# Kernel tuning notes

Hardware: AMD Instinct MI355X
Metric: run time of the kernel (lower is better)

## Reference

```python
import jax, jax.numpy as jnp
import numpy as np

B, N, D, D_OUT = 4, 512, 48, 48

def setup_inputs() -> dict:
    key = jax.random.key(0)
    ks = jax.random.split(key, 7)
    s1 = 1.0 / np.sqrt(2 * D)
    s2 = 1.0 / np.sqrt(2 * D)
    s3 = 1.0 / np.sqrt(D)
    return {
        "x": jax.random.normal(ks[0], (B, N, D), dtype=jnp.float32),
        "W1": jax.random.uniform(ks[1], (2 * D, 2 * D), jnp.float32, -s1, s1),
        "b1": jax.random.uniform(ks[2], (2 * D,), jnp.float32, -s1, s1),
        "W2": jax.random.uniform(ks[3], (2 * D, D), jnp.float32, -s2, s2),
        "b2": jax.random.uniform(ks[4], (D,), jnp.float32, -s2, s2),
        "W3": jax.random.uniform(ks[5], (D, D_OUT), jnp.float32, -s3, s3),
        "b3": jax.random.uniform(ks[6], (D_OUT,), jnp.float32, -s3, s3),
    }

def reference(x, W1, b1, W2, b2, W3, b3):
    # x: [B, N, D]
    Bn, Nn, Dn = x.shape
    xi = jnp.broadcast_to(x[:, :, None, :], (Bn, Nn, Nn, Dn))  # row i
    xj = jnp.broadcast_to(x[:, None, :, :], (Bn, Nn, Nn, Dn))  # col j
    pair = jnp.concatenate([xi, xj], axis=-1)  # [B,N,N,2D]
    h = jax.nn.gelu(pair @ W1 + b1, approximate=False)
    h = jax.nn.gelu(h @ W2 + b2, approximate=False)
    pair_out = h @ W3 + b3  # [B,N,N,d_out]
    mask = jnp.triu(jnp.ones((Nn, Nn), dtype=bool), 1)  # j > i masked
    pair_out = jnp.where(mask[None, :, :, None], 0.0, pair_out)
    w = jnp.linalg.norm(pair_out, axis=-1)  # [B,N,N]
    w = jnp.where(mask[None, :, :], -1e9, w)
    w = jax.nn.softmax(w, axis=-1)
    return jnp.einsum('bnj,bnjd->bnd', w, pair_out)
```

## Files before the change

### kernel.cpp

```cpp
#include <hip/hip_runtime.h>
#include <hip/hip_bf16.h>


constexpr int BATCH = 4;
constexpr int SEQ   = 512;
constexpr int DIM   = 48;
constexpr int DIM2  = 96;
constexpr int CH    = 64;

constexpr int AW  = 104;
constexpr int HW  = 72;

typedef short short8v __attribute__((ext_vector_type(8)));
typedef float float4v __attribute__((ext_vector_type(4)));
typedef unsigned int uint2v __attribute__((ext_vector_type(2)));

#define MFMA16(a, b, c) __builtin_amdgcn_mfma_f32_16x16x32_bf16(a, b, c, 0, 0, 0)

__device__ __forceinline__ float gelu_tanh(float x) {
    float u = x * x;
    float q = fmaf(0.10294537f, u, 2.3022077f);
    float e = __builtin_amdgcn_exp2f(x * q);
    float r = __builtin_amdgcn_rcpf(e + 1.0f);
    return fmaf(-x, r, x);
}
__device__ __forceinline__ short f2bf1(float v) {
    return (short)((__float_as_uint(v) + 0x8000u) >> 16);
}
__device__ __forceinline__ unsigned pack_bf16x2(float a, float b) {
    unsigned ua = __float_as_uint(a) + 0x8000u;
    unsigned ub = __float_as_uint(b) + 0x8000u;
    return __builtin_amdgcn_perm(ub, ua, 0x07060302u);
}
constexpr float LOG2E = 1.4426950408889634f;

__global__ __launch_bounds__(192) void uv_kernel(
    const float* __restrict__ x, const float* __restrict__ W1,
    const float* __restrict__ b1, float* __restrict__ U, float* __restrict__ V)
{
    __shared__ float sxT[DIM * 4];
    const int t = threadIdx.x;
    const int row0 = blockIdx.x * 4;
    if (t < DIM * 4) {
        int r = t / DIM, m = t - r * DIM;
        sxT[m * 4 + r] = x[(row0 + r) * DIM + m];
    }
    __syncthreads();
    const bool isU = (t < DIM2);
    const int  k   = isU ? t : (t - DIM2);
    const float* Wcol = W1 + (isU ? 0 : DIM * DIM2) + k;
    float binit = isU ? b1[k] : 0.0f;
    float a0 = binit, a1 = binit, a2 = binit, a3 = binit;
    #pragma unroll 8
    for (int m = 0; m < DIM; ++m) {
        float wv = Wcol[m * DIM2];
        const float4 xa = *(const float4*)&sxT[m * 4];
        a0 = fmaf(wv, xa.x, a0); a1 = fmaf(wv, xa.y, a1);
        a2 = fmaf(wv, xa.z, a2); a3 = fmaf(wv, xa.w, a3);
    }
    float* dst = isU ? U : V;
    dst[(row0 + 0) * DIM2 + k] = a0; dst[(row0 + 1) * DIM2 + k] = a1;
    dst[(row0 + 2) * DIM2 + k] = a2; dst[(row0 + 3) * DIM2 + k] = a3;
}

__global__ __launch_bounds__(256, 4) void pair_kernel(
    const float* __restrict__ U, const float* __restrict__ V,
    const float* __restrict__ W2, const float* __restrict__ b2,
    const float* __restrict__ W3, const float* __restrict__ b3,
    float* __restrict__ out)
{
    __shared__ __align__(16) char smem[23168];
    short* sA   = (short*)smem;
    short* sH   = (short*)(smem + 13312);
    float* sUi  = (float*)(smem + 22528);
    float* sNrm = (float*)(smem + 22912);

    const int t   = threadIdx.x;
    const int bid = blockIdx.x;
    const int b   = bid & (BATCH - 1);
    const int i   = (SEQ - 1) - (bid >> 2);
    const int rowbase = b * SEQ + i;

    const int lane = t & 63;
    const int w    = t >> 6;
    const int col  = lane & 15;
    const int quad = lane >> 4;
    const int qo   = quad * 8;
    const int m4   = w * 16 + col;
    const int rbase = w * 16 + quad * 4;

    for (int idx = t; idx < DIM2 * DIM; idx += 256) {
        int k = idx / DIM, n = idx - k * DIM;
        sA[n * AW + k] = f2bf1(W2[idx]);
    }
    for (int idx = t; idx < DIM * DIM; idx += 256) {
        int k = idx / DIM, n = idx - k * DIM;
        sH[n * HW + k] = f2bf1(W3[idx]);
    }
    for (int idx = t; idx < CH * 16; idx += 256)
        sH[(idx >> 4) * HW + 48 + (idx & 15)] = 0;
    if (t < DIM2) sUi[t] = U[rowbase * DIM2 + t];
    __syncthreads();

    const short* w2b = sA + col * AW + qo;
    const short8v w200 = *(const short8v*)(w2b + 0);
    const short8v w201 = *(const short8v*)(w2b + 32);
    const short8v w202 = *(const short8v*)(w2b + 64);
    const short8v w210 = *(const short8v*)(w2b + 16*AW + 0);
    const short8v w211 = *(const short8v*)(w2b + 16*AW + 32);
    const short8v w212 = *(const short8v*)(w2b + 16*AW + 64);
    const short8v w220 = *(const short8v*)(w2b + 32*AW + 0);
    const short8v w221 = *(const short8v*)(w2b + 32*AW + 32);
    const short8v w222 = *(const short8v*)(w2b + 32*AW + 64);
    const short* w3b = sH + col * HW + qo;
    const short8v w300 = *(const short8v*)(w3b + 0);
    const short8v w301 = *(const short8v*)(w3b + 32);
    const short8v w310 = *(const short8v*)(w3b + 16*HW + 0);
    const short8v w311 = *(const short8v*)(w3b + 16*HW + 32);
    const short8v w320 = *(const short8v*)(w3b + 32*HW + 0);
    const short8v w321 = *(const short8v*)(w3b + 32*HW + 32);
    const float bb20 = b2[col], bb21 = b2[16 + col], bb22 = b2[32 + col];
    const float bb30 = b3[col], bb31 = b3[16 + col], bb32 = b3[32 + col];
    __syncthreads();

    const int pr = t >> 2;
    const int pq = t & 3;

    float acc0 = 0.f, acc1 = 0.f, acc2 = 0.f;
    float m_run = -1e30f, l_run = 0.0f;

    for (int j0 = 0; j0 <= i; j0 += CH) {
        const int JJ = min(CH, i + 1 - j0);

        {
            const float* Vb = V + (b * SEQ + j0 + pr) * DIM2 + pq * 4;
            #pragma unroll
            for (int kk = 0; kk < 6; ++kk) {
                const float4 vv = *(const float4*)(Vb + 16 * kk);
                const float4 uu = *(const float4*)&sUi[(pq + 4 * kk) * 4];
                float g0 = gelu_tanh(uu.x + vv.x);
                float g1 = gelu_tanh(uu.y + vv.y);
                float g2 = gelu_tanh(uu.z + vv.z);
                float g3 = gelu_tanh(uu.w + vv.w);
                uint2v o;
                o.x = pack_bf16x2(g0, g1);
                o.y = pack_bf16x2(g2, g3);
                *(uint2v*)&sA[pr * AW + (pq + 4 * kk) * 4] = o;
            }
        }
        __syncthreads();

        {
            const short* arow = &sA[m4 * AW + qo];
            short8v a0 = *(const short8v*)(arow + 0);
            short8v a1 = *(const short8v*)(arow + 32);
            short8v a2 = *(const short8v*)(arow + 64);
            float4v c0 = {0.f,0.f,0.f,0.f}, c1 = c0, c2 = c0;
            c0 = MFMA16(a0, w200, c0); c0 = MFMA16(a1, w201, c0); c0 = MFMA16(a2, w202, c0);
            c1 = MFMA16(a0, w210, c1); c1 = MFMA16(a1, w211, c1); c1 = MFMA16(a2, w212, c1);
            c2 = MFMA16(a0, w220, c2); c2 = MFMA16(a1, w221, c2); c2 = MFMA16(a2, w222, c2);
            #pragma unroll
            for (int r = 0; r < 4; ++r) {
                sH[(rbase + r) * HW +  0 + col] = f2bf1(gelu_tanh(c0[r] + bb20));
                sH[(rbase + r) * HW + 16 + col] = f2bf1(gelu_tanh(c1[r] + bb21));
                sH[(rbase + r) * HW + 32 + col] = f2bf1(gelu_tanh(c2[r] + bb22));
            }
        }
        __syncthreads();

        float4v p0, p1, p2;
        {
            const short* hrw = &sH[m4 * HW + qo];
            short8v a0 = *(const short8v*)(hrw + 0);
            short8v a1 = *(const short8v*)(hrw + 32);
            float4v c0 = {0.f,0.f,0.f,0.f}, c1 = c0, c2 = c0;
            c0 = MFMA16(a0, w300, c0); c0 = MFMA16(a1, w301, c0);
            c1 = MFMA16(a0, w310, c1); c1 = MFMA16(a1, w311, c1);
            c2 = MFMA16(a0, w320, c2); c2 = MFMA16(a1, w321, c2);
            #pragma unroll
            for (int r = 0; r < 4; ++r) {
                p0[r] = c0[r] + bb30; p1[r] = c1[r] + bb31; p2[r] = c2[r] + bb32;
                float ss = p0[r]*p0[r] + p1[r]*p1[r] + p2[r]*p2[r];
                ss += __shfl_xor(ss, 1);
                ss += __shfl_xor(ss, 2);
                ss += __shfl_xor(ss, 4);
                ss += __shfl_xor(ss, 8);
                if (col == 0) sNrm[rbase + r] = sqrtf(ss);
            }
        }
        __syncthreads();

        {
            float nr = (lane < JJ) ? sNrm[lane] : -1e30f;
            float mx = nr;
            mx = fmaxf(mx, __shfl_xor(mx, 1));  mx = fmaxf(mx, __shfl_xor(mx, 2));
            mx = fmaxf(mx, __shfl_xor(mx, 4));  mx = fmaxf(mx, __shfl_xor(mx, 8));
            mx = fmaxf(mx, __shfl_xor(mx, 16)); mx = fmaxf(mx, __shfl_xor(mx, 32));
            float newm = fmaxf(m_run, mx);
            float e = (lane < JJ) ? __builtin_amdgcn_exp2f((nr - newm) * LOG2E) : 0.0f;
            float s = e;
            s += __shfl_xor(s, 1);  s += __shfl_xor(s, 2);
            s += __shfl_xor(s, 4);  s += __shfl_xor(s, 8);
            s += __shfl_xor(s, 16); s += __shfl_xor(s, 32);
            float sc = __builtin_amdgcn_exp2f((m_run - newm) * LOG2E);
            l_run = fmaf(l_run, sc, s);
            m_run = newm;
            acc0 *= sc; acc1 *= sc; acc2 *= sc;
            #pragma unroll
            for (int r = 0; r < 4; ++r) {
                float er = __shfl(e, rbase + r);
                acc0 = fmaf(er, p0[r], acc0);
                acc1 = fmaf(er, p1[r], acc1);
                acc2 = fmaf(er, p2[r], acc2);
            }
        }
    }

    acc0 += __shfl_xor(acc0, 16); acc0 += __shfl_xor(acc0, 32);
    acc1 += __shfl_xor(acc1, 16); acc1 += __shfl_xor(acc1, 32);
    acc2 += __shfl_xor(acc2, 16); acc2 += __shfl_xor(acc2, 32);
    float* sRed = (float*)sA;
    __syncthreads();
    if (lane < 16) {
        sRed[w * DIM + lane]      = acc0;
        sRed[w * DIM + 16 + lane] = acc1;
        sRed[w * DIM + 32 + lane] = acc2;
    }
    __syncthreads();
    if (t < DIM) {
        float o = (sRed[t] + sRed[DIM + t] + sRed[2*DIM + t] + sRed[3*DIM + t]) / l_run;
        out[rowbase * DIM + t] = o;
    }
}

extern "C" void kernel_launch(void* const* d_in, const int* in_sizes, int n_in,
                              void* d_out, int out_size, void* d_ws, size_t ws_size,
                              hipStream_t stream) {
    const float* x  = (const float*)d_in[0];
    const float* W1 = (const float*)d_in[1];
    const float* b1 = (const float*)d_in[2];
    const float* W2 = (const float*)d_in[3];
    const float* b2 = (const float*)d_in[4];
    const float* W3 = (const float*)d_in[5];
    const float* b3 = (const float*)d_in[6];
    float* out = (float*)d_out;

    float* U = (float*)d_ws;
    float* V = U + BATCH * SEQ * DIM2;

    uv_kernel<<<BATCH * SEQ / 4, 192, 0, stream>>>(x, W1, b1, U, V);
    pair_kernel<<<BATCH * SEQ, 256, 0, stream>>>(U, V, W2, b2, W3, b3, out);
}
```

Baseline: 114.9 us.

## Use per-wave online softmax, skip inactive waves, keep W2 in LDS

```diff
diff --git a/kernel.cpp b/kernel.cpp
--- a/kernel.cpp
+++ b/kernel.cpp
@@ -14,6 +14,7 @@
 typedef short short8v __attribute__((ext_vector_type(8)));
 typedef float float4v __attribute__((ext_vector_type(4)));
 typedef unsigned int uint2v __attribute__((ext_vector_type(2)));
+typedef unsigned int uint4v __attribute__((ext_vector_type(4)));
 
 #define MFMA16(a, b, c) __builtin_amdgcn_mfma_f32_16x16x32_bf16(a, b, c, 0, 0, 0)
 
@@ -63,17 +64,16 @@
     dst[(row0 + 2) * DIM2 + k] = a2; dst[(row0 + 3) * DIM2 + k] = a3;
 }
 
-__global__ __launch_bounds__(256, 4) void pair_kernel(
+__global__ __launch_bounds__(256, 5) void pair_kernel(
     const float* __restrict__ U, const float* __restrict__ V,
     const float* __restrict__ W2, const float* __restrict__ b2,
     const float* __restrict__ W3, const float* __restrict__ b3,
     float* __restrict__ out)
 {
-    __shared__ __align__(16) char smem[23168];
+    __shared__ __align__(16) char smem[32512];
     short* sA   = (short*)smem;
-    short* sH   = (short*)(smem + 13312);
-    float* sUi  = (float*)(smem + 22528);
-    float* sNrm = (float*)(smem + 22912);
+    short* sW2T = (short*)(smem + 13312);
+    short* sH   = (short*)(smem + 23296);
 
     const int t   = threadIdx.x;
     const int bid = blockIdx.x;
@@ -91,7 +91,7 @@
 
     for (int idx = t; idx < DIM2 * DIM; idx += 256) {
         int k = idx / DIM, n = idx - k * DIM;
-        sA[n * AW + k] = f2bf1(W2[idx]);
+        sW2T[n * AW + k] = f2bf1(W2[idx]);
     }
     for (int idx = t; idx < DIM * DIM; idx += 256) {
         int k = idx / DIM, n = idx - k * DIM;
@@ -99,19 +99,18 @@
     }
     for (int idx = t; idx < CH * 16; idx += 256)
         sH[(idx >> 4) * HW + 48 + (idx & 15)] = 0;
-    if (t < DIM2) sUi[t] = U[rowbase * DIM2 + t];
-    __syncthreads();
-
-    const short* w2b = sA + col * AW + qo;
-    const short8v w200 = *(const short8v*)(w2b + 0);
-    const short8v w201 = *(const short8v*)(w2b + 32);
-    const short8v w202 = *(const short8v*)(w2b + 64);
-    const short8v w210 = *(const short8v*)(w2b + 16*AW + 0);
-    const short8v w211 = *(const short8v*)(w2b + 16*AW + 32);
-    const short8v w212 = *(const short8v*)(w2b + 16*AW + 64);
-    const short8v w220 = *(const short8v*)(w2b + 32*AW + 0);
-    const short8v w221 = *(const short8v*)(w2b + 32*AW + 32);
-    const short8v w222 = *(const short8v*)(w2b + 32*AW + 64);
+    {
+        uint4v z = {0u, 0u, 0u, 0u};
+        for (int idx = t; idx < (CH * AW * 2) / 16; idx += 256)
+            ((uint4v*)sA)[idx] = z;
+    }
+    const int pr = t >> 2;
+    const int pq = t & 3;
+    float4 uu[6];
+    #pragma unroll
+    for (int k = 0; k < 6; ++k) uu[k] = *(const float4*)&U[rowbase * DIM2 + (pq + 4 * k) * 4];
+    __syncthreads();
+
     const short* w3b = sH + col * HW + qo;
     const short8v w300 = *(const short8v*)(w3b + 0);
     const short8v w301 = *(const short8v*)(w3b + 32);
@@ -123,25 +122,22 @@
     const float bb30 = b3[col], bb31 = b3[16 + col], bb32 = b3[32 + col];
     __syncthreads();
 
-    const int pr = t >> 2;
-    const int pq = t & 3;
-
     float acc0 = 0.f, acc1 = 0.f, acc2 = 0.f;
     float m_run = -1e30f, l_run = 0.0f;
 
     for (int j0 = 0; j0 <= i; j0 += CH) {
-        const int JJ = min(CH, i + 1 - j0);
-
-        {
+        const int jmax = i - j0;
+        const bool active = ((w << 4) <= jmax);
+
+        if (active) {
             const float* Vb = V + (b * SEQ + j0 + pr) * DIM2 + pq * 4;
             #pragma unroll
             for (int kk = 0; kk < 6; ++kk) {
                 const float4 vv = *(const float4*)(Vb + 16 * kk);
-                const float4 uu = *(const float4*)&sUi[(pq + 4 * kk) * 4];
-                float g0 = gelu_tanh(uu.x + vv.x);
-                float g1 = gelu_tanh(uu.y + vv.y);
-                float g2 = gelu_tanh(uu.z + vv.z);
-                float g3 = gelu_tanh(uu.w + vv.w);
+                float g0 = gelu_tanh(uu[kk].x + vv.x);
+                float g1 = gelu_tanh(uu[kk].y + vv.y);
+                float g2 = gelu_tanh(uu[kk].z + vv.z);
+                float g3 = gelu_tanh(uu[kk].w + vv.w);
                 uint2v o;
                 o.x = pack_bf16x2(g0, g1);
                 o.y = pack_bf16x2(g2, g3);
@@ -150,15 +146,22 @@
         }
         __syncthreads();
 
-        {
+        if (active) {
             const short* arow = &sA[m4 * AW + qo];
             short8v a0 = *(const short8v*)(arow + 0);
             short8v a1 = *(const short8v*)(arow + 32);
             short8v a2 = *(const short8v*)(arow + 64);
+            const short* w2b = sW2T + col * AW + qo;
             float4v c0 = {0.f,0.f,0.f,0.f}, c1 = c0, c2 = c0;
-            c0 = MFMA16(a0, w200, c0); c0 = MFMA16(a1, w201, c0); c0 = MFMA16(a2, w202, c0);
-            c1 = MFMA16(a0, w210, c1); c1 = MFMA16(a1, w211, c1); c1 = MFMA16(a2, w212, c1);
-            c2 = MFMA16(a0, w220, c2); c2 = MFMA16(a1, w221, c2); c2 = MFMA16(a2, w222, c2);
+            c0 = MFMA16(a0, *(const short8v*)(w2b + 0),          c0);
+            c0 = MFMA16(a1, *(const short8v*)(w2b + 32),         c0);
+            c0 = MFMA16(a2, *(const short8v*)(w2b + 64),         c0);
+            c1 = MFMA16(a0, *(const short8v*)(w2b + 16*AW + 0),  c1);
+            c1 = MFMA16(a1, *(const short8v*)(w2b + 16*AW + 32), c1);
+            c1 = MFMA16(a2, *(const short8v*)(w2b + 16*AW + 64), c1);
+            c2 = MFMA16(a0, *(const short8v*)(w2b + 32*AW + 0),  c2);
+            c2 = MFMA16(a1, *(const short8v*)(w2b + 32*AW + 32), c2);
+            c2 = MFMA16(a2, *(const short8v*)(w2b + 32*AW + 64), c2);
             #pragma unroll
             for (int r = 0; r < 4; ++r) {
                 sH[(rbase + r) * HW +  0 + col] = f2bf1(gelu_tanh(c0[r] + bb20));
@@ -168,8 +171,7 @@
         }
         __syncthreads();
 
-        float4v p0, p1, p2;
-        {
+        if (active) {
             const short* hrw = &sH[m4 * HW + qo];
             short8v a0 = *(const short8v*)(hrw + 0);
             short8v a1 = *(const short8v*)(hrw + 32);
@@ -177,6 +179,8 @@
             c0 = MFMA16(a0, w300, c0); c0 = MFMA16(a1, w301, c0);
             c1 = MFMA16(a0, w310, c1); c1 = MFMA16(a1, w311, c1);
             c2 = MFMA16(a0, w320, c2); c2 = MFMA16(a1, w321, c2);
+            float4v p0, p1, p2;
+            float vr[4];
             #pragma unroll
             for (int r = 0; r < 4; ++r) {
                 p0[r] = c0[r] + bb30; p1[r] = c1[r] + bb31; p2[r] = c2[r] + bb32;
@@ -185,51 +189,53 @@
                 ss += __shfl_xor(ss, 2);
                 ss += __shfl_xor(ss, 4);
                 ss += __shfl_xor(ss, 8);
-                if (col == 0) sNrm[rbase + r] = sqrtf(ss);
+                vr[r] = (rbase + r <= jmax) ? __builtin_amdgcn_sqrtf(ss) : -1e30f;
             }
-        }
-        __syncthreads();
-
-        {
-            float nr = (lane < JJ) ? sNrm[lane] : -1e30f;
-            float mx = nr;
-            mx = fmaxf(mx, __shfl_xor(mx, 1));  mx = fmaxf(mx, __shfl_xor(mx, 2));
-            mx = fmaxf(mx, __shfl_xor(mx, 4));  mx = fmaxf(mx, __shfl_xor(mx, 8));
-            mx = fmaxf(mx, __shfl_xor(mx, 16)); mx = fmaxf(mx, __shfl_xor(mx, 32));
-            float newm = fmaxf(m_run, mx);
-            float e = (lane < JJ) ? __builtin_amdgcn_exp2f((nr - newm) * LOG2E) : 0.0f;
-            float s = e;
-            s += __shfl_xor(s, 1);  s += __shfl_xor(s, 2);
-            s += __shfl_xor(s, 4);  s += __shfl_xor(s, 8);
-            s += __shfl_xor(s, 16); s += __shfl_xor(s, 32);
+            float mloc = fmaxf(fmaxf(vr[0], vr[1]), fmaxf(vr[2], vr[3]));
+            mloc = fmaxf(mloc, __shfl_xor(mloc, 16));
+            mloc = fmaxf(mloc, __shfl_xor(mloc, 32));
+            float newm = fmaxf(m_run, mloc);
             float sc = __builtin_amdgcn_exp2f((m_run - newm) * LOG2E);
+            float e0 = __builtin_amdgcn_exp2f((vr[0] - newm) * LOG2E);
+            float e1 = __builtin_amdgcn_exp2f((vr[1] - newm) * LOG2E);
+            float e2 = __builtin_amdgcn_exp2f((vr[2] - newm) * LOG2E);
+            float e3 = __builtin_amdgcn_exp2f((vr[3] - newm) * LOG2E);
+            float s = (e0 + e1) + (e2 + e3);
+            s += __shfl_xor(s, 16);
+            s += __shfl_xor(s, 32);
             l_run = fmaf(l_run, sc, s);
             m_run = newm;
             acc0 *= sc; acc1 *= sc; acc2 *= sc;
-            #pragma unroll
-            for (int r = 0; r < 4; ++r) {
-                float er = __shfl(e, rbase + r);
-                acc0 = fmaf(er, p0[r], acc0);
-                acc1 = fmaf(er, p1[r], acc1);
-                acc2 = fmaf(er, p2[r], acc2);
-            }
+            acc0 = fmaf(e0, p0[0], acc0); acc1 = fmaf(e0, p1[0], acc1); acc2 = fmaf(e0, p2[0], acc2);
+            acc0 = fmaf(e1, p0[1], acc0); acc1 = fmaf(e1, p1[1], acc1); acc2 = fmaf(e1, p2[1], acc2);
+            acc0 = fmaf(e2, p0[2], acc0); acc1 = fmaf(e2, p1[2], acc1); acc2 = fmaf(e2, p2[2], acc2);
+            acc0 = fmaf(e3, p0[3], acc0); acc1 = fmaf(e3, p1[3], acc1); acc2 = fmaf(e3, p2[3], acc2);
         }
     }
 
     acc0 += __shfl_xor(acc0, 16); acc0 += __shfl_xor(acc0, 32);
     acc1 += __shfl_xor(acc1, 16); acc1 += __shfl_xor(acc1, 32);
     acc2 += __shfl_xor(acc2, 16); acc2 += __shfl_xor(acc2, 32);
-    float* sRed = (float*)sA;
+    float* red = (float*)smem;
     __syncthreads();
     if (lane < 16) {
-        sRed[w * DIM + lane]      = acc0;
-        sRed[w * DIM + 16 + lane] = acc1;
-        sRed[w * DIM + 32 + lane] = acc2;
-    }
+        red[w * 64 + lane]      = acc0;
+        red[w * 64 + 16 + lane] = acc1;
+        red[w * 64 + 32 + lane] = acc2;
+    }
+    if (lane == 0) { red[w * 64 + 48] = m_run; red[w * 64 + 49] = l_run; }
     __syncthreads();
     if (t < DIM) {
-        float o = (sRed[t] + sRed[DIM + t] + sRed[2*DIM + t] + sRed[3*DIM + t]) / l_run;
-        out[rowbase * DIM + t] = o;
+        float mm0 = red[48],       mm1 = red[64 + 48];
+        float mm2 = red[128 + 48], mm3 = red[192 + 48];
+        float M = fmaxf(fmaxf(mm0, mm1), fmaxf(mm2, mm3));
+        float f0 = __builtin_amdgcn_exp2f((mm0 - M) * LOG2E);
+        float f1 = __builtin_amdgcn_exp2f((mm1 - M) * LOG2E);
+        float f2 = __builtin_amdgcn_exp2f((mm2 - M) * LOG2E);
+        float f3 = __builtin_amdgcn_exp2f((mm3 - M) * LOG2E);
+        float num = f0 * red[t] + f1 * red[64 + t] + f2 * red[128 + t] + f3 * red[192 + t];
+        float den = f0 * red[49] + f1 * red[64 + 49] + f2 * red[128 + 49] + f3 * red[192 + 49];
+        out[rowbase * DIM + t] = num / den;
     }
 }
 
```

After: 123.9 us. 7.8% more time.
